# Kernel tuning notes

Hardware: AMD Instinct MI355X
Metric: run time of the kernel (lower is better)

The kernel has to match this reference:

```python
import jax, jax.numpy as jnp
import numpy as np
from jax import lax

T, B, D = 128, 64, 64  # time steps, batch, embed_dim


def setup_inputs() -> dict:
    key = jax.random.key(0)
    k1, k2, k3, k4, k5 = jax.random.split(key, 5)
    scale = 1.0 / np.sqrt(D)
    return {
        "data_r": jax.random.normal(k1, (T, B, D, D), dtype=jnp.float32) * scale,
        "data_i": jax.random.normal(k2, (T, B, D, D), dtype=jnp.float32) * scale,
        "U_r": jax.random.normal(k3, (D, D), dtype=jnp.float32) * scale,
        "U_i": jax.random.normal(k4, (D, D), dtype=jnp.float32) * scale,
        "lam": jax.random.uniform(k5, (), dtype=jnp.float32),
    }


def reference(data_r, data_i, U_r, U_i, lam):
    """QRNN forward. Original loops num_layers times but every layer shares the
    same cell (ModuleList([cell]*L)) and re-consumes the raw `data`, overwriting
    in_states -- so the result equals a single-layer scan, computed here once.

    QRNNCell (reconstructed): complex density-matrix update
        v  = sigmoid(lam) * h + (1 - sigmoid(lam)) * x          (complex mix)
        h' = U v U^H                                            (unitary evolution)
    with h0 = eye(D)/D (maximally mixed state), h0_i = 0.
    """
    g = jax.nn.sigmoid(lam)
    U_rT, U_iT = U_r.T, U_i.T

    def step(h, x):
        h_r, h_i = h
        x_r, x_i = x
        # complex convex mix of hidden state and input density matrix
        v_r = g * h_r + (1.0 - g) * x_r  # [B, D, D]
        v_i = g * h_i + (1.0 - g) * x_i
        # t = U @ v   (complex):  U is [D,D], v is [B,D,D]
        t_r = jnp.einsum('pq,bqr->bpr', U_r, v_r) - jnp.einsum('pq,bqr->bpr', U_i, v_i)
        t_i = jnp.einsum('pq,bqr->bpr', U_r, v_i) + jnp.einsum('pq,bqr->bpr', U_i, v_r)
        # h' = t @ U^H, with U^H = U_r.T - i U_i.T
        hn_r = t_r @ U_rT + t_i @ U_iT
        hn_i = t_i @ U_rT - t_r @ U_iT
        return (hn_r, hn_i), (hn_r, hn_i)

    h0_r = jnp.broadcast_to(jnp.eye(D, dtype=data_r.dtype) / D, (B, D, D))
    h0_i = jnp.zeros_like(h0_r)
    _, (all_r, all_i) = lax.scan(step, (h0_r, h0_i), (data_r, data_i))
    # list of [h_r, h_i] per time step -> stacked [2, T, B, D, D]
    return jnp.stack([all_r, all_i])
```

## Files before the change

### kernel.cpp

```cpp
#include <hip/hip_runtime.h>
#include <math.h>

typedef _Float16 half8 __attribute__((ext_vector_type(8)));
typedef _Float16 half4_t __attribute__((ext_vector_type(4)));
typedef float floatx16 __attribute__((ext_vector_type(16)));
typedef float float4_t __attribute__((ext_vector_type(4)));

#define NT 128
#define NB 64
#define NC 8
#define CL 16

typedef __attribute__((address_space(1))) float gfloat;
typedef __attribute__((address_space(1))) float4_t gfloat4;
__device__ __forceinline__ float4_t gload4(const float* p) {
  return *(const gfloat4*)(unsigned long long)p;
}
__device__ __forceinline__ float gload1(const float* p) {
  return *(const gfloat*)(unsigned long long)p;
}
__device__ __forceinline__ void gstore4(float* p, float4_t v) {
  *(gfloat4*)(unsigned long long)p = v;
}
__device__ __forceinline__ void gstore1(float* p, float v) {
  *(gfloat*)(unsigned long long)p = v;
}

__device__ __forceinline__ int eidx(int row, int col) {
  return row * 64 + ((((col >> 3) ^ row) & 7) << 3) + (col & 7);
}
__device__ __forceinline__ int uidx(int row, int cb) { return (cb * 64 + row) * 8; }
__device__ __forceinline__ int jcolf(int j, int pblk, int hi) {
  return 32 * pblk + (j & 3) + 8 * (j >> 2) + 4 * hi;
}

__device__ __forceinline__ void alpha_from_max(float mm, float& alpha, float& alphainv) {
  unsigned eb = (__float_as_uint(mm) >> 23) & 0xFFu;
  eb = (eb == 0u) ? 126u : eb;
  alpha    = __uint_as_float((253u - eb) << 23);
  alphainv = __uint_as_float((eb + 1u) << 23);
}

#define BARX() do {                                        \
  asm volatile("s_waitcnt lgkmcnt(0)" ::: "memory");       \
  __builtin_amdgcn_s_barrier();                            \
  __builtin_amdgcn_sched_barrier(0);                       \
} while (0)

template<bool PASS3>
__global__ __launch_bounds__(512, 4)
void qrnn_scan(const float* __restrict__ data_r, const float* __restrict__ data_i,
               const float* __restrict__ U_r, const float* __restrict__ U_i,
               const float* __restrict__ lam_p, float* __restrict__ out) {
  __shared__ __align__(16) _Float16 Uhr[4096], Uhi_[4096], Ulr[4096], Uli_[4096];
  __shared__ __align__(16) _Float16 Vr[4096], Vi[4096];
  __shared__ __align__(16) _Float16 Tr[4096], Ti[4096];
  __shared__ __align__(16) float red[8];

  const int bx = blockIdx.x;
  const int b  = bx & (NB - 1);
  const int c  = bx >> 6;
  const int t0 = c * CL;
  const int tid = threadIdx.x;
  const int lane = tid & 63, hi = lane >> 5, l31 = lane & 31, w = tid >> 6;
  const int grp = w >> 2, rblk = (w >> 1) & 1, pblk = w & 1;
  const int prow = 32 * rblk + l31;
  const int urow = 32 * pblk + l31;

  const float g = 1.0f / (1.0f + expf(-lam_p[0]));

  const int dq = tid >> 3, cb0 = tid & 7, dr0 = cb0 * 8;
  {
    const float4_t a0 = gload4(U_r + dq * 64 + dr0);
    const float4_t a1 = gload4(U_r + dq * 64 + dr0 + 4);
    const float4_t b0 = gload4(U_i + dq * 64 + dr0);
    const float4_t b1 = gload4(U_i + dq * 64 + dr0 + 4);
    half8 hr, lr, hm, lm;
    #pragma unroll
    for (int e = 0; e < 4; ++e) {
      _Float16 h;
      h = (_Float16)a0[e]; hr[e]     = h; lr[e]     = (_Float16)((a0[e] - (float)h) * 256.0f);
      h = (_Float16)a1[e]; hr[4 + e] = h; lr[4 + e] = (_Float16)((a1[e] - (float)h) * 256.0f);
      h = (_Float16)b0[e]; hm[e]     = h; lm[e]     = (_Float16)((b0[e] - (float)h) * 256.0f);
      h = (_Float16)b1[e]; hm[4 + e] = h; lm[4 + e] = (_Float16)((b1[e] - (float)h) * 256.0f);
    }
    const int off = uidx(dq, cb0);
    *(half8*)&Uhr[off]  = hr;  *(half8*)&Ulr[off]  = lr;
    *(half8*)&Uhi_[off] = hm;  *(half8*)&Uli_[off] = lm;
  }

  float rv[16];
  if constexpr (PASS3) {
    if (c == 0) {
      #pragma unroll
      for (int j = 0; j < 16; ++j)
        rv[j] = (grp == 0 && prow == jcolf(j, pblk, hi)) ? (1.0f / 64.0f) : 0.0f;
    } else {
      const float* hs = out + ((size_t)((grp ? NT : 0) + t0 + 1) * NB + b) * 4096;
      #pragma unroll
      for (int j = 0; j < 16; ++j)
        rv[j] = gload1(hs + prow * 64 + jcolf(j, pblk, hi));
    }
  } else {
    #pragma unroll
    for (int j = 0; j < 16; ++j) rv[j] = 0.0f;
  }
  {
    float ml = 0.0f;
    #pragma unroll
    for (int j = 0; j < 16; ++j) ml = fmaxf(ml, fabsf(rv[j]));
    #pragma unroll
    for (int d = 32; d >= 1; d >>= 1) ml = fmaxf(ml, __shfl_xor(ml, d, 64));
    if (lane == 0) red[w] = ml;
  }

  const float* __restrict__ xsrc = grp ? data_i : data_r;
  const size_t xoff = (size_t)prow * 64 + 32 * pblk + 4 * hi;
  float4_t px[4];
  {
    const float* xp = xsrc + ((size_t)t0 * NB + b) * 4096 + xoff;
    #pragma unroll
    for (int jj = 0; jj < 4; ++jj) px[jj] = gload4(xp + 8 * jj);
  }
  BARX();

  float Sig, alpha = 1.0f, alphainv = 1.0f;
  {
    float4_t r0 = *(const float4_t*)&red[0];
    float4_t r1 = *(const float4_t*)&red[4];
    float mm = fmaxf(fmaxf(fmaxf(r0[0], r0[1]), fmaxf(r0[2], r0[3])),
                     fmaxf(fmaxf(r1[0], r1[1]), fmaxf(r1[2], r1[3])));
    float sc;
    alpha_from_max(mm, sc, Sig);
    #pragma unroll
    for (int j = 0; j < 16; ++j) rv[j] *= sc;
  }

  for (int s = 0; s < CL; ++s) {
    {
      const float ga = g * alpha;
      const float kx = (1.0f - g) * alpha / Sig;
      _Float16* Vg = grp ? Vi : Vr;
      #pragma unroll
      for (int jj = 0; jj < 4; ++jj) {
        const int j0 = 32 * pblk + 8 * jj + 4 * hi;
        #pragma unroll
        for (int e = 0; e < 4; ++e) {
          const float vv = ga * rv[4 * jj + e] + kx * px[jj][e];
          Vg[eidx(j0 + e, prow)] = (_Float16)vv;
        }
      }
      float m0[8];
      #pragma unroll
      for (int e = 0; e < 8; ++e) m0[e] = fmaxf(fabsf(rv[e]), fabsf(rv[e + 8]));
      #pragma unroll
      for (int e = 0; e < 4; ++e) m0[e] = fmaxf(m0[e], m0[e + 4]);
      float ml = fmaxf(fmaxf(m0[0], m0[1]), fmaxf(m0[2], m0[3]));
      #pragma unroll
      for (int d = 32; d >= 1; d >>= 1) ml = fmaxf(ml, __shfl_xor(ml, d, 64));
      if (lane == 0) red[w] = ml;
    }
    BARX();

    if (s + 1 < CL) {
      const float* xp = xsrc + ((size_t)(t0 + s + 1) * NB + b) * 4096 + xoff;
      #pragma unroll
      for (int jj = 0; jj < 4; ++jj) px[jj] = gload4(xp + 8 * jj);
    }
    if constexpr (PASS3) {
      if (s > 0) {
        float* oR = out + ((size_t)(t0 + s - 1) * NB + b) * 4096
                        + (grp ? (size_t)NT * NB * 4096 : 0) + (size_t)(prow * 64);
        #pragma unroll
        for (int jj = 0; jj < 4; ++jj) {
          const int j0 = 32 * pblk + 8 * jj + 4 * hi;
          float4_t ov;
          #pragma unroll
          for (int e = 0; e < 4; ++e) ov[e] = Sig * rv[4 * jj + e];
          gstore4(oR + j0, ov);
        }
      }
    }
    Sig *= alphainv;
    {
      float4_t r0 = *(const float4_t*)&red[0];
      float4_t r1 = *(const float4_t*)&red[4];
      float mm = fmaxf(fmaxf(fmaxf(r0[0], r0[1]), fmaxf(r0[2], r0[3])),
                       fmaxf(fmaxf(r1[0], r1[1]), fmaxf(r1[2], r1[3])));
      alpha_from_max(mm, alpha, alphainv);
    }

    {
      floatx16 ah, al;
      #pragma unroll
      for (int j = 0; j < 16; ++j) { ah[j] = 0.0f; al[j] = 0.0f; }
      #pragma unroll
      for (int kq = 0; kq < 4; ++kq) {
        const int cc = 16 * kq + 8 * hi;
        const int vo = eidx(prow, cc);
        const int uo = uidx(urow, 2 * kq + hi);
        half8 avr = *(const half8*)&Vr[vo];
        half8 avi = *(const half8*)&Vi[vo];
        half8 f0 = grp ? avi : avr;
        half8 f1 = grp ? avr : -avi;
        ah = __builtin_amdgcn_mfma_f32_32x32x16_f16(f0, *(const half8*)&Uhr[uo], ah, 0, 0, 0);
        ah = __builtin_amdgcn_mfma_f32_32x32x16_f16(f1, *(const half8*)&Uhi_[uo], ah, 0, 0, 0);
        al = __builtin_amdgcn_mfma_f32_32x32x16_f16(f0, *(const half8*)&Ulr[uo], al, 0, 0, 0);
        al = __builtin_amdgcn_mfma_f32_32x32x16_f16(f1, *(const half8*)&Uli_[uo], al, 0, 0, 0);
      }
      _Float16* Tg = grp ? Ti : Tr;
      const int tp = 32 * pblk + l31;
      #pragma unroll
      for (int jj = 0; jj < 4; ++jj) {
        const int rr0 = 32 * rblk + 8 * jj + 4 * hi;
        half4_t tv;
        #pragma unroll
        for (int e = 0; e < 4; ++e) {
          const int j = 4 * jj + e;
          tv[e] = (_Float16)(ah[j] + al[j] * 0.00390625f);
        }
        *(half4_t*)&Tg[eidx(tp, rr0)] = tv;
      }
    }
    BARX();

    {
      floatx16 ch, cl;
      #pragma unroll
      for (int j = 0; j < 16; ++j) { ch[j] = 0.0f; cl[j] = 0.0f; }
      const int p2 = 32 * rblk + l31;
      #pragma unroll
      for (int kq = 0; kq < 4; ++kq) {
        const int cc = 16 * kq + 8 * hi;
        const int to = eidx(p2, cc);
        const int uo = uidx(urow, 2 * kq + hi);
        half8 btr = *(const half8*)&Tr[to];
        half8 bti = *(const half8*)&Ti[to];
        half8 f0 = grp ? bti : btr;
        half8 f1 = grp ? -btr : bti;
        ch = __builtin_amdgcn_mfma_f32_32x32x16_f16(*(const half8*)&Uhr[uo], f0, ch, 0, 0, 0);
        ch = __builtin_amdgcn_mfma_f32_32x32x16_f16(*(const half8*)&Uhi_[uo], f1, ch, 0, 0, 0);
        cl = __builtin_amdgcn_mfma_f32_32x32x16_f16(*(const half8*)&Ulr[uo], f0, cl, 0, 0, 0);
        cl = __builtin_amdgcn_mfma_f32_32x32x16_f16(*(const half8*)&Uli_[uo], f1, cl, 0, 0, 0);
      }
      #pragma unroll
      for (int j = 0; j < 16; ++j)
        rv[j] = ch[j] + cl[j] * 0.00390625f;
    }
  }

  {
    const int trow = PASS3 ? (t0 + CL - 1) : t0;
    float* eR = out + ((size_t)trow * NB + b) * 4096
                    + (grp ? (size_t)NT * NB * 4096 : 0) + (size_t)(prow * 64);
    #pragma unroll
    for (int jj = 0; jj < 4; ++jj) {
      const int j0 = 32 * pblk + 8 * jj + 4 * hi;
      float4_t ov;
      #pragma unroll
      for (int e = 0; e < 4; ++e) ov[e] = Sig * rv[4 * jj + e];
      gstore4(eR + j0, ov);
    }
  }
}

__global__ __launch_bounds__(512, 1)
void qrnn_combine(const float* __restrict__ U_r, const float* __restrict__ U_i,
                  const float* __restrict__ lam_p, float* __restrict__ out) {
  __shared__ float Ga_r[64 * 68], Ga_i[64 * 68], Gb_r[64 * 68], Gb_i[64 * 68];
  __shared__ __align__(16) _Float16 Vr[4096], Vi[4096], Tr[4096], Ti[4096];
  __shared__ float red[8];

  const int b = blockIdx.x;
  const int tid = threadIdx.x;
  const int lane = tid & 63, hi = lane >> 5, l31 = lane & 31, w = tid >> 6;
  const int grp = w >> 2, rblk = (w >> 1) & 1, pblk = w & 1;
  const int prow = 32 * rblk + l31;

  const float g = 1.0f / (1.0f + expf(-lam_p[0]));
  const float g2 = g * g, g4 = g2 * g2, g8 = g4 * g4, g16 = g8 * g8;

  const int qr = tid >> 3, qc = (tid & 7) * 8;
  {
    *(float4_t*)&Ga_r[qr * 68 + qc]     = gload4(U_r + qr * 64 + qc);
    *(float4_t*)&Ga_r[qr * 68 + qc + 4] = gload4(U_r + qr * 64 + qc + 4);
    *(float4_t*)&Ga_i[qr * 68 + qc]     = gload4(U_i + qr * 64 + qc);
    *(float4_t*)&Ga_i[qr * 68 + qc + 4] = gload4(U_i + qr * 64 + qc + 4);
  }
  __syncthreads();

  #pragma unroll
  for (int it = 0; it < 4; ++it) {
    const float* sr = (it & 1) ? Gb_r : Ga_r;
    const float* si = (it & 1) ? Gb_i : Ga_i;
    float* dr = (it & 1) ? Ga_r : Gb_r;
    float* di = (it & 1) ? Ga_i : Gb_i;
    float cr[8], ci[8];
    #pragma unroll
    for (int e = 0; e < 8; ++e) { cr[e] = 0.0f; ci[e] = 0.0f; }
    for (int k = 0; k < 64; ++k) {
      const float ar = sr[qr * 68 + k];
      const float ai = si[qr * 68 + k];
      float4_t br0 = *(const float4_t*)&sr[k * 68 + qc];
      float4_t br1 = *(const float4_t*)&sr[k * 68 + qc + 4];
      float4_t bi0 = *(const float4_t*)&si[k * 68 + qc];
      float4_t bi1 = *(const float4_t*)&si[k * 68 + qc + 4];
      #pragma unroll
      for (int e = 0; e < 4; ++e) {
        cr[e]     += ar * br0[e] - ai * bi0[e];
        ci[e]     += ar * bi0[e] + ai * br0[e];
        cr[4 + e] += ar * br1[e] - ai * bi1[e];
        ci[4 + e] += ar * bi1[e] + ai * br1[e];
      }
    }
    float4_t s0, s1, s2, s3;
    #pragma unroll
    for (int e = 0; e < 4; ++e) { s0[e] = cr[e]; s1[e] = cr[4 + e]; s2[e] = ci[e]; s3[e] = ci[4 + e]; }
    *(float4_t*)&dr[qr * 68 + qc] = s0;  *(float4_t*)&dr[qr * 68 + qc + 4] = s1;
    *(float4_t*)&di[qr * 68 + qc] = s2;  *(float4_t*)&di[qr * 68 + qc + 4] = s3;
    __syncthreads();
  }

  half8 Wrh[4], Wrl[4], Wih[4], Wil[4];
  {
    const int row = 32 * pblk + l31;
    #pragma unroll
    for (int kq = 0; kq < 4; ++kq) {
      const int c0 = 16 * kq + 8 * hi;
      #pragma unroll
      for (int e = 0; e < 8; ++e) {
        const float wr = Ga_r[row * 68 + c0 + e];
        const float wi = Ga_i[row * 68 + c0 + e];
        _Float16 h;
        h = (_Float16)wr; Wrh[kq][e] = h; Wrl[kq][e] = (_Float16)((wr - (float)h) * 256.0f);
        h = (_Float16)wi; Wih[kq][e] = h; Wil[kq][e] = (_Float16)((wi - (float)h) * 256.0f);
      }
    }
  }

  float rv[16];
  #pragma unroll
  for (int j = 0; j < 16; ++j)
    rv[j] = (grp == 0 && prow == jcolf(j, pblk, hi)) ? (1.0f / 64.0f) : 0.0f;

  for (int c = 0; c < NC - 1; ++c) {
    float pv[16];
    {
      const float* ps = out + ((size_t)((grp ? NT : 0) + c * CL) * NB + b) * 4096;
      #pragma unroll
      for (int j = 0; j < 16; ++j) pv[j] = gload1(ps + prow * 64 + jcolf(j, pblk, hi));
    }
    float ml = 0.0f;
    #pragma unroll
    for (int j = 0; j < 16; ++j) ml = fmaxf(ml, fabsf(rv[j]));
    #pragma unroll
    for (int d = 32; d >= 1; d >>= 1) ml = fmaxf(ml, __shfl_xor(ml, d, 64));
    if (lane == 0) red[w] = ml;
    __syncthreads();
    float mm = red[0];
    #pragma unroll
    for (int i = 1; i < 8; ++i) mm = fmaxf(mm, red[i]);
    float al, alinv;
    alpha_from_max(mm, al, alinv);
    const float fE = g16 * alinv;

    {
      _Float16* Vg = grp ? Vi : Vr;
      #pragma unroll
      for (int j = 0; j < 16; ++j)
        Vg[eidx(jcolf(j, pblk, hi), prow)] = (_Float16)(al * rv[j]);
    }
    __syncthreads();

    {
      half8 A0[4], A1[4];
      const int rrow = 32 * rblk + l31;
      #pragma unroll
      for (int kq = 0; kq < 4; ++kq) {
        const int cc = 16 * kq + 8 * hi;
        half8 avr = *(const half8*)&Vr[eidx(rrow, cc)];
        half8 avi = *(const half8*)&Vi[eidx(rrow, cc)];
        if (grp == 0) { A0[kq] = avr; A1[kq] = avi; }
        else          { A0[kq] = avi; A1[kq] = avr; }
      }
      floatx16 a1h, a1l, a2h, a2l;
      #pragma unroll
      for (int j = 0; j < 16; ++j) { a1h[j] = 0; a1l[j] = 0; a2h[j] = 0; a2l[j] = 0; }
      #pragma unroll
      for (int kq = 0; kq < 4; ++kq) {
        a1h = __builtin_amdgcn_mfma_f32_32x32x16_f16(A0[kq], Wrh[kq], a1h, 0, 0, 0);
        a2h = __builtin_amdgcn_mfma_f32_32x32x16_f16(A1[kq], Wih[kq], a2h, 0, 0, 0);
        a1l = __builtin_amdgcn_mfma_f32_32x32x16_f16(A0[kq], Wrl[kq], a1l, 0, 0, 0);
        a2l = __builtin_amdgcn_mfma_f32_32x32x16_f16(A1[kq], Wil[kq], a2l, 0, 0, 0);
      }
      const float s1 = grp ? 1.0f : -1.0f;
      _Float16* Tg = grp ? Ti : Tr;
      const int tp = 32 * pblk + l31;
      #pragma unroll
      for (int jj = 0; jj < 4; ++jj) {
        const int rr0 = 32 * rblk + 8 * jj + 4 * hi;
        half4_t tv;
        #pragma unroll
        for (int e = 0; e < 4; ++e) {
          const int j = 4 * jj + e;
          tv[e] = (_Float16)((a1h[j] + s1 * a2h[j]) + (a1l[j] + s1 * a2l[j]) * 0.00390625f);
        }
        *(half4_t*)&Tg[eidx(tp, rr0)] = tv;
      }
    }
    __syncthreads();

    {
      half8 B0[4], B1[4];
      const int p2 = 32 * rblk + l31;
      #pragma unroll
      for (int kq = 0; kq < 4; ++kq) {
        const int cc = 16 * kq + 8 * hi;
        half8 btr = *(const half8*)&Tr[eidx(p2, cc)];
        half8 bti = *(const half8*)&Ti[eidx(p2, cc)];
        if (grp == 0) { B0[kq] = btr; B1[kq] = bti; }
        else          { B0[kq] = bti; B1[kq] = btr; }
      }
      floatx16 c1h, c1l, c2h, c2l;
      #pragma unroll
      for (int j = 0; j < 16; ++j) { c1h[j] = 0; c1l[j] = 0; c2h[j] = 0; c2l[j] = 0; }
      #pragma unroll
      for (int kq = 0; kq < 4; ++kq) {
        c1h = __builtin_amdgcn_mfma_f32_32x32x16_f16(Wrh[kq], B0[kq], c1h, 0, 0, 0);
        c2h = __builtin_amdgcn_mfma_f32_32x32x16_f16(Wih[kq], B1[kq], c2h, 0, 0, 0);
        c1l = __builtin_amdgcn_mfma_f32_32x32x16_f16(Wrl[kq], B0[kq], c1l, 0, 0, 0);
        c2l = __builtin_amdgcn_mfma_f32_32x32x16_f16(Wil[kq], B1[kq], c2l, 0, 0, 0);
      }
      const float s2 = grp ? -1.0f : 1.0f;
      #pragma unroll
      for (int j = 0; j < 16; ++j) {
        const float rvS = (c1h[j] + s2 * c2h[j]) + (c1l[j] + s2 * c2l[j]) * 0.00390625f;
        rv[j] = fE * rvS + pv[j];
      }
    }
    {
      float* hs = out + ((size_t)((grp ? NT : 0) + (c + 1) * CL + 1) * NB + b) * 4096;
      #pragma unroll
      for (int j = 0; j < 16; ++j) gstore1(hs + prow * 64 + jcolf(j, pblk, hi), rv[j]);
    }
    __syncthreads();
  }
}

extern "C" void kernel_launch(void* const* d_in, const int* in_sizes, int n_in,
                              void* d_out, int out_size, void* d_ws, size_t ws_size,
                              hipStream_t stream) {
  (void)in_sizes; (void)n_in; (void)out_size; (void)d_ws; (void)ws_size;
  const float* dr = (const float*)d_in[0];
  const float* di = (const float*)d_in[1];
  const float* ur = (const float*)d_in[2];
  const float* ui = (const float*)d_in[3];
  const float* lm = (const float*)d_in[4];
  float* o = (float*)d_out;
  qrnn_scan<false><<<dim3(NB * NC), dim3(512), 0, stream>>>(dr, di, ur, ui, lm, o);
  qrnn_combine<<<dim3(NB), dim3(512), 0, stream>>>(ur, ui, lm, o);
  qrnn_scan<true><<<dim3(NB * NC), dim3(512), 0, stream>>>(dr, di, ur, ui, lm, o);
}
```

Baseline: 289.1 us.

## Keep U fragments in registers and fold split-precision MFMAs into one accumulator

Moves the fp16 hi/lo split of U out of shared memory and into per-lane registers, so the per-step LDS reads of U disappear. The low-part products are folded into the same accumulator by pre-scaling the operand by 1/256 in fp16, and the same single-accumulator form is applied to the second kernel's MFMA chains. This drops the extra accumulator arrays and the combine arithmetic. Prefetched inputs are kept as fp16 instead of fp32 to cut register use. The trade-offs are more VGPRs held for U, extra fp16 multiplies, and lost precision from scaling small values in fp16 and rounding x early.

```diff
diff --git a/kernel.cpp b/kernel.cpp
--- a/kernel.cpp
+++ b/kernel.cpp
@@ -29,9 +29,16 @@
 __device__ __forceinline__ int eidx(int row, int col) {
   return row * 64 + ((((col >> 3) ^ row) & 7) << 3) + (col & 7);
 }
-__device__ __forceinline__ int uidx(int row, int cb) { return (cb * 64 + row) * 8; }
 __device__ __forceinline__ int jcolf(int j, int pblk, int hi) {
   return 32 * pblk + (j & 3) + 8 * (j >> 2) + 4 * hi;
+}
+
+__device__ __forceinline__ half8 hscale8(half8 v) {
+  const _Float16 s = (_Float16)0.00390625f;
+  half8 r;
+  #pragma unroll
+  for (int e = 0; e < 8; ++e) r[e] = v[e] * s;
+  return r;
 }
 
 __device__ __forceinline__ void alpha_from_max(float mm, float& alpha, float& alphainv) {
@@ -52,7 +59,6 @@
 void qrnn_scan(const float* __restrict__ data_r, const float* __restrict__ data_i,
                const float* __restrict__ U_r, const float* __restrict__ U_i,
                const float* __restrict__ lam_p, float* __restrict__ out) {
-  __shared__ __align__(16) _Float16 Uhr[4096], Uhi_[4096], Ulr[4096], Uli_[4096];
   __shared__ __align__(16) _Float16 Vr[4096], Vi[4096];
   __shared__ __align__(16) _Float16 Tr[4096], Ti[4096];
   __shared__ __align__(16) float red[8];
@@ -65,28 +71,28 @@
   const int lane = tid & 63, hi = lane >> 5, l31 = lane & 31, w = tid >> 6;
   const int grp = w >> 2, rblk = (w >> 1) & 1, pblk = w & 1;
   const int prow = 32 * rblk + l31;
-  const int urow = 32 * pblk + l31;
 
   const float g = 1.0f / (1.0f + expf(-lam_p[0]));
 
-  const int dq = tid >> 3, cb0 = tid & 7, dr0 = cb0 * 8;
-  {
-    const float4_t a0 = gload4(U_r + dq * 64 + dr0);
-    const float4_t a1 = gload4(U_r + dq * 64 + dr0 + 4);
-    const float4_t b0 = gload4(U_i + dq * 64 + dr0);
-    const float4_t b1 = gload4(U_i + dq * 64 + dr0 + 4);
-    half8 hr, lr, hm, lm;
-    #pragma unroll
-    for (int e = 0; e < 4; ++e) {
-      _Float16 h;
-      h = (_Float16)a0[e]; hr[e]     = h; lr[e]     = (_Float16)((a0[e] - (float)h) * 256.0f);
-      h = (_Float16)a1[e]; hr[4 + e] = h; lr[4 + e] = (_Float16)((a1[e] - (float)h) * 256.0f);
-      h = (_Float16)b0[e]; hm[e]     = h; lm[e]     = (_Float16)((b0[e] - (float)h) * 256.0f);
-      h = (_Float16)b1[e]; hm[4 + e] = h; lm[4 + e] = (_Float16)((b1[e] - (float)h) * 256.0f);
-    }
-    const int off = uidx(dq, cb0);
-    *(half8*)&Uhr[off]  = hr;  *(half8*)&Ulr[off]  = lr;
-    *(half8*)&Uhi_[off] = hm;  *(half8*)&Uli_[off] = lm;
+  half8 Urh[4], Url[4], Uih[4], Uil[4];
+  {
+    const int row = 32 * pblk + l31;
+    #pragma unroll
+    for (int kq = 0; kq < 4; ++kq) {
+      const int c0 = 16 * kq + 8 * hi;
+      const float4_t a0 = gload4(U_r + row * 64 + c0);
+      const float4_t a1 = gload4(U_r + row * 64 + c0 + 4);
+      const float4_t b0 = gload4(U_i + row * 64 + c0);
+      const float4_t b1 = gload4(U_i + row * 64 + c0 + 4);
+      #pragma unroll
+      for (int e = 0; e < 4; ++e) {
+        _Float16 h;
+        h = (_Float16)a0[e]; Urh[kq][e]     = h; Url[kq][e]     = (_Float16)((a0[e] - (float)h) * 256.0f);
+        h = (_Float16)a1[e]; Urh[kq][4 + e] = h; Url[kq][4 + e] = (_Float16)((a1[e] - (float)h) * 256.0f);
+        h = (_Float16)b0[e]; Uih[kq][e]     = h; Uil[kq][e]     = (_Float16)((b0[e] - (float)h) * 256.0f);
+        h = (_Float16)b1[e]; Uih[kq][4 + e] = h; Uil[kq][4 + e] = (_Float16)((b1[e] - (float)h) * 256.0f);
+      }
+    }
   }
 
   float rv[16];
@@ -116,11 +122,15 @@
 
   const float* __restrict__ xsrc = grp ? data_i : data_r;
   const size_t xoff = (size_t)prow * 64 + 32 * pblk + 4 * hi;
-  float4_t px[4];
+  half4_t pxh[4];
   {
     const float* xp = xsrc + ((size_t)t0 * NB + b) * 4096 + xoff;
     #pragma unroll
-    for (int jj = 0; jj < 4; ++jj) px[jj] = gload4(xp + 8 * jj);
+    for (int jj = 0; jj < 4; ++jj) {
+      const float4_t t = gload4(xp + 8 * jj);
+      #pragma unroll
+      for (int e = 0; e < 4; ++e) pxh[jj][e] = (_Float16)t[e];
+    }
   }
   BARX();
 
@@ -146,7 +156,7 @@
         const int j0 = 32 * pblk + 8 * jj + 4 * hi;
         #pragma unroll
         for (int e = 0; e < 4; ++e) {
-          const float vv = ga * rv[4 * jj + e] + kx * px[jj][e];
+          const float vv = ga * rv[4 * jj + e] + kx * (float)pxh[jj][e];
           Vg[eidx(j0 + e, prow)] = (_Float16)vv;
         }
       }
@@ -165,7 +175,11 @@
     if (s + 1 < CL) {
       const float* xp = xsrc + ((size_t)(t0 + s + 1) * NB + b) * 4096 + xoff;
       #pragma unroll
-      for (int jj = 0; jj < 4; ++jj) px[jj] = gload4(xp + 8 * jj);
+      for (int jj = 0; jj < 4; ++jj) {
+        const float4_t t = gload4(xp + 8 * jj);
+        #pragma unroll
+        for (int e = 0; e < 4; ++e) pxh[jj][e] = (_Float16)t[e];
+      }
     }
     if constexpr (PASS3) {
       if (s > 0) {
@@ -191,22 +205,21 @@
     }
 
     {
-      floatx16 ah, al;
-      #pragma unroll
-      for (int j = 0; j < 16; ++j) { ah[j] = 0.0f; al[j] = 0.0f; }
+      floatx16 ah;
+      #pragma unroll
+      for (int j = 0; j < 16; ++j) ah[j] = 0.0f;
       #pragma unroll
       for (int kq = 0; kq < 4; ++kq) {
         const int cc = 16 * kq + 8 * hi;
         const int vo = eidx(prow, cc);
-        const int uo = uidx(urow, 2 * kq + hi);
         half8 avr = *(const half8*)&Vr[vo];
         half8 avi = *(const half8*)&Vi[vo];
         half8 f0 = grp ? avi : avr;
         half8 f1 = grp ? avr : -avi;
-        ah = __builtin_amdgcn_mfma_f32_32x32x16_f16(f0, *(const half8*)&Uhr[uo], ah, 0, 0, 0);
-        ah = __builtin_amdgcn_mfma_f32_32x32x16_f16(f1, *(const half8*)&Uhi_[uo], ah, 0, 0, 0);
-        al = __builtin_amdgcn_mfma_f32_32x32x16_f16(f0, *(const half8*)&Ulr[uo], al, 0, 0, 0);
-        al = __builtin_amdgcn_mfma_f32_32x32x16_f16(f1, *(const half8*)&Uli_[uo], al, 0, 0, 0);
+        ah = __builtin_amdgcn_mfma_f32_32x32x16_f16(f0, Urh[kq], ah, 0, 0, 0);
+        ah = __builtin_amdgcn_mfma_f32_32x32x16_f16(f1, Uih[kq], ah, 0, 0, 0);
+        ah = __builtin_amdgcn_mfma_f32_32x32x16_f16(hscale8(f0), Url[kq], ah, 0, 0, 0);
+        ah = __builtin_amdgcn_mfma_f32_32x32x16_f16(hscale8(f1), Uil[kq], ah, 0, 0, 0);
       }
       _Float16* Tg = grp ? Ti : Tr;
       const int tp = 32 * pblk + l31;
@@ -215,37 +228,32 @@
         const int rr0 = 32 * rblk + 8 * jj + 4 * hi;
         half4_t tv;
         #pragma unroll
-        for (int e = 0; e < 4; ++e) {
-          const int j = 4 * jj + e;
-          tv[e] = (_Float16)(ah[j] + al[j] * 0.00390625f);
-        }
+        for (int e = 0; e < 4; ++e) tv[e] = (_Float16)ah[4 * jj + e];
         *(half4_t*)&Tg[eidx(tp, rr0)] = tv;
       }
     }
     BARX();
 
     {
-      floatx16 ch, cl;
-      #pragma unroll
-      for (int j = 0; j < 16; ++j) { ch[j] = 0.0f; cl[j] = 0.0f; }
+      floatx16 ch;
+      #pragma unroll
+      for (int j = 0; j < 16; ++j) ch[j] = 0.0f;
       const int p2 = 32 * rblk + l31;
       #pragma unroll
       for (int kq = 0; kq < 4; ++kq) {
         const int cc = 16 * kq + 8 * hi;
         const int to = eidx(p2, cc);
-        const int uo = uidx(urow, 2 * kq + hi);
         half8 btr = *(const half8*)&Tr[to];
         half8 bti = *(const half8*)&Ti[to];
         half8 f0 = grp ? bti : btr;
         half8 f1 = grp ? -btr : bti;
-        ch = __builtin_amdgcn_mfma_f32_32x32x16_f16(*(const half8*)&Uhr[uo], f0, ch, 0, 0, 0);
-        ch = __builtin_amdgcn_mfma_f32_32x32x16_f16(*(const half8*)&Uhi_[uo], f1, ch, 0, 0, 0);
-        cl = __builtin_amdgcn_mfma_f32_32x32x16_f16(*(const half8*)&Ulr[uo], f0, cl, 0, 0, 0);
-        cl = __builtin_amdgcn_mfma_f32_32x32x16_f16(*(const half8*)&Uli_[uo], f1, cl, 0, 0, 0);
-      }
-      #pragma unroll
-      for (int j = 0; j < 16; ++j)
-        rv[j] = ch[j] + cl[j] * 0.00390625f;
+        ch = __builtin_amdgcn_mfma_f32_32x32x16_f16(Urh[kq], f0, ch, 0, 0, 0);
+        ch = __builtin_amdgcn_mfma_f32_32x32x16_f16(Uih[kq], f1, ch, 0, 0, 0);
+        ch = __builtin_amdgcn_mfma_f32_32x32x16_f16(Url[kq], hscale8(f0), ch, 0, 0, 0);
+        ch = __builtin_amdgcn_mfma_f32_32x32x16_f16(Uil[kq], hscale8(f1), ch, 0, 0, 0);
+      }
+      #pragma unroll
+      for (int j = 0; j < 16; ++j) rv[j] = ch[j];
     }
   }
 
@@ -373,27 +381,22 @@
     __syncthreads();
 
     {
-      half8 A0[4], A1[4];
+      floatx16 ah;
+      #pragma unroll
+      for (int j = 0; j < 16; ++j) ah[j] = 0.0f;
       const int rrow = 32 * rblk + l31;
       #pragma unroll
       for (int kq = 0; kq < 4; ++kq) {
         const int cc = 16 * kq + 8 * hi;
         half8 avr = *(const half8*)&Vr[eidx(rrow, cc)];
         half8 avi = *(const half8*)&Vi[eidx(rrow, cc)];
-        if (grp == 0) { A0[kq] = avr; A1[kq] = avi; }
-        else          { A0[kq] = avi; A1[kq] = avr; }
-      }
-      floatx16 a1h, a1l, a2h, a2l;
-      #pragma unroll
-      for (int j = 0; j < 16; ++j) { a1h[j] = 0; a1l[j] = 0; a2h[j] = 0; a2l[j] = 0; }
-      #pragma unroll
-      for (int kq = 0; kq < 4; ++kq) {
-        a1h = __builtin_amdgcn_mfma_f32_32x32x16_f16(A0[kq], Wrh[kq], a1h, 0, 0, 0);
-        a2h = __builtin_amdgcn_mfma_f32_32x32x16_f16(A1[kq], Wih[kq], a2h, 0, 0, 0);
-        a1l = __builtin_amdgcn_mfma_f32_32x32x16_f16(A0[kq], Wrl[kq], a1l, 0, 0, 0);
-        a2l = __builtin_amdgcn_mfma_f32_32x32x16_f16(A1[kq], Wil[kq], a2l, 0, 0, 0);
-      }
-      const float s1 = grp ? 1.0f : -1.0f;
+        half8 f0 = grp ? avi : avr;
+        half8 f1 = grp ? avr : -avi;
+        ah = __builtin_amdgcn_mfma_f32_32x32x16_f16(f0, Wrh[kq], ah, 0, 0, 0);
+        ah = __builtin_amdgcn_mfma_f32_32x32x16_f16(f1, Wih[kq], ah, 0, 0, 0);
+        ah = __builtin_amdgcn_mfma_f32_32x32x16_f16(hscale8(f0), Wrl[kq], ah, 0, 0, 0);
+        ah = __builtin_amdgcn_mfma_f32_32x32x16_f16(hscale8(f1), Wil[kq], ah, 0, 0, 0);
+      }
       _Float16* Tg = grp ? Ti : Tr;
       const int tp = 32 * pblk + l31;
       #pragma unroll
@@ -401,42 +404,31 @@
         const int rr0 = 32 * rblk + 8 * jj + 4 * hi;
         half4_t tv;
         #pragma unroll
-        for (int e = 0; e < 4; ++e) {
-          const int j = 4 * jj + e;
-          tv[e] = (_Float16)((a1h[j] + s1 * a2h[j]) + (a1l[j] + s1 * a2l[j]) * 0.00390625f);
-        }
+        for (int e = 0; e < 4; ++e) tv[e] = (_Float16)ah[4 * jj + e];
         *(half4_t*)&Tg[eidx(tp, rr0)] = tv;
       }
     }
     __syncthreads();
 
     {
-      half8 B0[4], B1[4];
+      floatx16 ch;
+      #pragma unroll
+      for (int j = 0; j < 16; ++j) ch[j] = 0.0f;
       const int p2 = 32 * rblk + l31;
       #pragma unroll
       for (int kq = 0; kq < 4; ++kq) {
         const int cc = 16 * kq + 8 * hi;
         half8 btr = *(const half8*)&Tr[eidx(p2, cc)];
         half8 bti = *(const half8*)&Ti[eidx(p2, cc)];
-        if (grp == 0) { B0[kq] = btr; B1[kq] = bti; }
-        else          { B0[kq] = bti; B1[kq] = btr; }
-      }
-      floatx16 c1h, c1l, c2h, c2l;
-      #pragma unroll
-      for (int j = 0; j < 16; ++j) { c1h[j] = 0; c1l[j] = 0; c2h[j] = 0; c2l[j] = 0; }
-      #pragma unroll
-      for (int kq = 0; kq < 4; ++kq) {
-        c1h = __builtin_amdgcn_mfma_f32_32x32x16_f16(Wrh[kq], B0[kq], c1h, 0, 0, 0);
-        c2h = __builtin_amdgcn_mfma_f32_32x32x16_f16(Wih[kq], B1[kq], c2h, 0, 0, 0);
-        c1l = __builtin_amdgcn_mfma_f32_32x32x16_f16(Wrl[kq], B0[kq], c1l, 0, 0, 0);
-        c2l = __builtin_amdgcn_mfma_f32_32x32x16_f16(Wil[kq], B1[kq], c2l, 0, 0, 0);
-      }
-      const float s2 = grp ? -1.0f : 1.0f;
-      #pragma unroll
-      for (int j = 0; j < 16; ++j) {
-        const float rvS = (c1h[j] + s2 * c2h[j]) + (c1l[j] + s2 * c2l[j]) * 0.00390625f;
-        rv[j] = fE * rvS + pv[j];
-      }
+        half8 f0 = grp ? bti : btr;
+        half8 f1 = grp ? -btr : bti;
+        ch = __builtin_amdgcn_mfma_f32_32x32x16_f16(Wrh[kq], f0, ch, 0, 0, 0);
+        ch = __builtin_amdgcn_mfma_f32_32x32x16_f16(Wih[kq], f1, ch, 0, 0, 0);
+        ch = __builtin_amdgcn_mfma_f32_32x32x16_f16(Wrl[kq], hscale8(f0), ch, 0, 0, 0);
+        ch = __builtin_amdgcn_mfma_f32_32x32x16_f16(Wil[kq], hscale8(f1), ch, 0, 0, 0);
+      }
+      #pragma unroll
+      for (int j = 0; j < 16; ++j) rv[j] = fE * ch[j] + pv[j];
     }
     {
       float* hs = out + ((size_t)((grp ? NT : 0) + (c + 1) * CL + 1) * NB + b) * 4096;
```

After: 370.9 us. +28.3%, slower.
